# Kernel tuning notes

Measured on AMD Instinct MI355X. Metric: run time of the kernel, lower is better.

Reference implementation:

```python
import jax, jax.numpy as jnp
import numpy as np

BN_EPS = 1e-5


def setup_inputs() -> dict:
    key = jax.random.key(0)
    k1, k2, k3 = jax.random.split(key, 3)
    n, d = 4096, 128
    x = jax.random.normal(k1, (2 * n, d), dtype=jnp.float32)
    affinity_A = jax.random.normal(k2, (n, n), dtype=jnp.float32)
    # Xavier-uniform-like init for the [d, d] weight
    lim = float(np.sqrt(6.0 / (d + d)))
    weight = jax.random.uniform(k3, (d, d), dtype=jnp.float32, minval=-lim, maxval=lim)
    gamma = jnp.ones((d,), dtype=jnp.float32)
    beta = jnp.zeros((d,), dtype=jnp.float32)
    return {"x": x, "affinity_A": affinity_A, "weight": weight, "gamma": gamma, "beta": beta}


def reference(x, affinity_A, weight, gamma, beta):
    # Binarize affinity
    A = jnp.where(affinity_A > 0, 1.0, 0.0).astype(x.dtype)  # [n, n]
    n = A.shape[0]
    I = jnp.eye(n, dtype=x.dtype)
    # Block adjacency [[A, I], [I, A]] -> [2n, 2n]
    adj = jnp.block([[A, I], [I, A]])
    # Symmetric normalization D^{-1/2} A D^{-1/2}.
    # (Original code materializes D^{-1/2} as a full matrix and does two O(n^3)
    # matmuls; mathematically it is just row/column scaling, done here directly.)
    deg = adj.sum(axis=1)                 # [2n], >= 1 because of identity blocks
    dinv = deg ** -0.5
    norm_A = dinv[:, None] * adj * dinv[None, :]
    # GCN propagation: (norm_A @ x) @ W
    h = (norm_A @ x) @ weight             # [2n, d]
    # BatchNorm1d (training mode, biased variance) + ReLU
    mean = h.mean(axis=0)
    var = h.var(axis=0)
    h = (h - mean) * jax.lax.rsqrt(var + BN_EPS) * gamma + beta
    return jax.nn.relu(h)
```

## Files before the change

### kernel.cpp

```cpp
#include <hip/hip_runtime.h>
#include <stdint.h>


#define N_NODES 4096
#define D 128
#define TWO_N (2*N_NODES)

typedef unsigned short u16;
typedef __bf16 bf16;
typedef bf16 bf16x8 __attribute__((ext_vector_type(8)));
typedef float f32x4 __attribute__((ext_vector_type(4)));
typedef u16 u16x8 __attribute__((ext_vector_type(8)));

__device__ __forceinline__ float bf2f(u16 u) {
    return __builtin_bit_cast(float, ((unsigned)u) << 16);
}
__device__ __forceinline__ u16 f2bf(float f) {
    unsigned b = __builtin_bit_cast(unsigned, f);
    unsigned r = (b + 0x7FFFu + ((b >> 16) & 1u)) >> 16;
    return (u16)r;
}
__device__ __forceinline__ bool det_fp32(const u16* gamma) {
    return gamma[0] != (u16)0x3F80;
}

__global__ void k_degscale(const void* __restrict__ x, const void* __restrict__ aff,
                           const void* __restrict__ W, const u16* __restrict__ gamma,
                           float* __restrict__ dinv, u16* __restrict__ XsT,
                           u16* __restrict__ WT) {
    int t = threadIdx.x;
    bool fp32 = det_fp32(gamma);
    const u16* W16 = (const u16*)W;
    const float* W32 = (const float*)W;

    if (blockIdx.x >= 256) {
        int o = (blockIdx.x - 256) * 16 + (t >> 4);
        int cg = (t & 15) * 8;
        u16x8 wv;
        #pragma unroll
        for (int e = 0; e < 8; ++e) {
            size_t wi = (size_t)(cg + e) * D + o;
            float v = fp32 ? W32[wi] : bf2f(W16[wi]);
            wv[e] = f2bf(v);
        }
        *reinterpret_cast<u16x8*>(WT + (size_t)o * D + cg) = wv;
        return;
    }

    __shared__ int scnt[16];
    __shared__ float sdinv[16];
    int wid = t >> 6, lane = t & 63;
    int j0 = blockIdx.x * 16;

    int cnt[4] = {0, 0, 0, 0};
    if (!fp32) {
        const u16* base = (const u16*)aff + (size_t)(j0 + wid * 4) * N_NODES;
        #pragma unroll
        for (int r = 0; r < 4; ++r)
            #pragma unroll
            for (int k = 0; k < 8; ++k) {
                u16x8 v = *reinterpret_cast<const u16x8*>(base + (size_t)r * N_NODES + k * 512 + lane * 8);
                #pragma unroll
                for (int e = 0; e < 8; ++e) cnt[r] += ((short)v[e] > 0) ? 1 : 0;
            }
    } else {
        const float* base = (const float*)aff + (size_t)(j0 + wid * 4) * N_NODES;
        #pragma unroll
        for (int r = 0; r < 4; ++r)
            #pragma unroll
            for (int k = 0; k < 16; ++k) {
                f32x4 v = *reinterpret_cast<const f32x4*>(base + (size_t)r * N_NODES + k * 256 + lane * 4);
                #pragma unroll
                for (int e = 0; e < 4; ++e) cnt[r] += (v[e] > 0.f) ? 1 : 0;
            }
    }
    #pragma unroll
    for (int r = 0; r < 4; ++r) {
        int c = cnt[r];
        #pragma unroll
        for (int off = 32; off; off >>= 1) c += __shfl_down(c, off, 64);
        if (lane == 0) scnt[wid * 4 + r] = c;
    }
    __syncthreads();
    if (t < 16) {
        float d = rsqrtf((float)(scnt[t] + 1));
        sdinv[t] = d;
        dinv[j0 + t] = d;
    }
    __syncthreads();

    int cc = t & 127;
    const u16* xb16 = (const u16*)x + ((t < 128) ? (size_t)0 : (size_t)N_NODES * D);
    const float* xb32 = (const float*)x + ((t < 128) ? (size_t)0 : (size_t)N_NODES * D);
    u16x8 b0, b1;
    #pragma unroll
    for (int jl = 0; jl < 8; ++jl) {
        size_t xi = (size_t)(j0 + jl) * D + cc;
        float xv = fp32 ? xb32[xi] : bf2f(xb16[xi]);
        b0[jl] = f2bf(sdinv[jl] * xv);
    }
    #pragma unroll
    for (int jl = 0; jl < 8; ++jl) {
        size_t xi = (size_t)(j0 + 8 + jl) * D + cc;
        float xv = fp32 ? xb32[xi] : bf2f(xb16[xi]);
        b1[jl] = f2bf(sdinv[8 + jl] * xv);
    }
    *reinterpret_cast<u16x8*>(XsT + (size_t)t * N_NODES + j0) = b0;
    *reinterpret_cast<u16x8*>(XsT + (size_t)t * N_NODES + j0 + 8) = b1;
}

#define BM 32
#define BN 256
#define BK 64
#define SK 4
#define KCHUNK (N_NODES / SK)
#define LDSS 68

__launch_bounds__(256, 2)
__global__ void k_gemm(const void* __restrict__ aff, const u16* __restrict__ XsT,
                       const u16* __restrict__ gamma, u16* __restrict__ Ypart) {
    __shared__ u16 sA[BM * LDSS];
    __shared__ u16 sB[BN * LDSS];
    int tid = threadIdx.x;
    bool fp32 = det_fp32(gamma);
    int mt = blockIdx.x >> 2;
    int sk = blockIdx.x & 3;
    int rm0 = mt * BM;
    int kk0 = sk * KCHUNK;
    int lane = tid & 63, wid = tid >> 6;
    int quad = lane >> 4, l15 = lane & 15;

    f32x4 acc[2][4];
    #pragma unroll
    for (int i = 0; i < 2; ++i)
        #pragma unroll
        for (int j = 0; j < 4; ++j) acc[i][j] = (f32x4){0.f, 0.f, 0.f, 0.f};

    int arow = tid >> 3;
    int acol = (tid & 7) * 8;
    const u16* agp16 = (const u16*)aff + (size_t)(rm0 + arow) * N_NODES + kk0 + acol;
    const float* agp32 = (const float*)aff + (size_t)(rm0 + arow) * N_NODES + kk0 + acol;
    int brow0 = tid >> 3;
    int bcol = (tid & 7) * 8;
    const u16* bgp = XsT + (size_t)brow0 * N_NODES + kk0 + bcol;

    u16x8 pa16; f32x4 pa32a, pa32b;
    u16x8 pb[8];

    if (!fp32) pa16 = *reinterpret_cast<const u16x8*>(agp16);
    else { pa32a = *reinterpret_cast<const f32x4*>(agp32); pa32b = *reinterpret_cast<const f32x4*>(agp32 + 4); }
    #pragma unroll
    for (int p = 0; p < 8; ++p)
        pb[p] = *reinterpret_cast<const u16x8*>(bgp + (size_t)p * 32 * N_NODES);

    for (int kk = 0; kk < KCHUNK / BK; ++kk) {
        u16x8 ab;
        if (!fp32) {
            #pragma unroll
            for (int e = 0; e < 8; ++e) ab[e] = ((short)pa16[e] > 0) ? (u16)0x3F80 : (u16)0;
        } else {
            #pragma unroll
            for (int e = 0; e < 4; ++e) {
                ab[e]     = (pa32a[e] > 0.f) ? (u16)0x3F80 : (u16)0;
                ab[4 + e] = (pa32b[e] > 0.f) ? (u16)0x3F80 : (u16)0;
            }
        }
        __syncthreads();
        *reinterpret_cast<u16x8*>(sA + arow * LDSS + acol) = ab;
        #pragma unroll
        for (int p = 0; p < 8; ++p)
            *reinterpret_cast<u16x8*>(sB + (p * 32 + brow0) * LDSS + bcol) = pb[p];
        __syncthreads();

        if (kk < KCHUNK / BK - 1) {
            int off = (kk + 1) * BK;
            if (!fp32) pa16 = *reinterpret_cast<const u16x8*>(agp16 + off);
            else { pa32a = *reinterpret_cast<const f32x4*>(agp32 + off); pa32b = *reinterpret_cast<const f32x4*>(agp32 + off + 4); }
            #pragma unroll
            for (int p = 0; p < 8; ++p)
                pb[p] = *reinterpret_cast<const u16x8*>(bgp + (size_t)p * 32 * N_NODES + off);
        }

        #pragma unroll
        for (int ks = 0; ks < 2; ++ks) {
            bf16x8 af0 = *reinterpret_cast<const bf16x8*>(sA + l15 * LDSS + ks * 32 + quad * 8);
            bf16x8 af1 = *reinterpret_cast<const bf16x8*>(sA + (16 + l15) * LDSS + ks * 32 + quad * 8);
            #pragma unroll
            for (int j = 0; j < 4; ++j) {
                bf16x8 bfr = *reinterpret_cast<const bf16x8*>(sB + (wid * 64 + j * 16 + l15) * LDSS + ks * 32 + quad * 8);
                acc[0][j] = __builtin_amdgcn_mfma_f32_16x16x32_bf16(af0, bfr, acc[0][j], 0, 0, 0);
                acc[1][j] = __builtin_amdgcn_mfma_f32_16x16x32_bf16(af1, bfr, acc[1][j], 0, 0, 0);
            }
        }
    }

    u16* yp = Ypart + (size_t)sk * N_NODES * 256;
    #pragma unroll
    for (int i = 0; i < 2; ++i) {
        int row = rm0 + i * 16 + quad * 4;
        #pragma unroll
        for (int j = 0; j < 4; ++j) {
            int col = wid * 64 + j * 16 + l15;
            #pragma unroll
            for (int r = 0; r < 4; ++r)
                yp[(size_t)(row + r) * 256 + col] = f2bf(acc[i][j][r]);
        }
    }
}

__global__ void k_comb(const u16* __restrict__ Ypart, const void* __restrict__ x,
                       const u16* __restrict__ WT, const u16* __restrict__ gamma,
                       const float* __restrict__ dinv, u16* __restrict__ hpre,
                       float* __restrict__ pS, float* __restrict__ pQ) {
    __shared__ u16 sH[32 * 136];
    __shared__ u16 sWT[128 * 136];
    __shared__ float sOut[32 * 132];
    int t = threadIdx.x;
    bool fp32 = det_fp32(gamma);
    int r0 = blockIdx.x * 32;
    bool top = blockIdx.x < 128;
    int node0 = top ? r0 : r0 - N_NODES;
    const u16* x16 = (const u16*)x;
    const float* x32 = (const float*)x;

    #pragma unroll
    for (int p = 0; p < 2; ++p) {
        int r = (t >> 4) + p * 16;
        int c0 = (t & 15) * 8;
        int node = node0 + r;
        int ycol = (top ? 0 : 128) + c0;
        float fs[8] = {0.f, 0.f, 0.f, 0.f, 0.f, 0.f, 0.f, 0.f};
        #pragma unroll
        for (int sk = 0; sk < SK; ++sk) {
            u16x8 yv = *reinterpret_cast<const u16x8*>(Ypart + ((size_t)sk * N_NODES + node) * 256 + ycol);
            #pragma unroll
            for (int e = 0; e < 8; ++e) fs[e] += bf2f(yv[e]);
        }
        float dv = dinv[node];
        size_t xi = (top ? (size_t)(N_NODES + node) : (size_t)node) * D + c0;
        u16x8 hv;
        if (!fp32) {
            u16x8 xv = *reinterpret_cast<const u16x8*>(x16 + xi);
            #pragma unroll
            for (int e = 0; e < 8; ++e) hv[e] = f2bf(dv * fs[e] + dv * dv * bf2f(xv[e]));
        } else {
            f32x4 xa = *reinterpret_cast<const f32x4*>(x32 + xi);
            f32x4 xb = *reinterpret_cast<const f32x4*>(x32 + xi + 4);
            #pragma unroll
            for (int e = 0; e < 4; ++e) {
                hv[e]     = f2bf(dv * fs[e]     + dv * dv * xa[e]);
                hv[4 + e] = f2bf(dv * fs[4 + e] + dv * dv * xb[e]);
            }
        }
        *reinterpret_cast<u16x8*>(sH + r * 136 + c0) = hv;
    }
    #pragma unroll
    for (int p = 0; p < 8; ++p) {
        int idx = p * 256 + t;
        int o = idx >> 4;
        int cg = (idx & 15) * 8;
        u16x8 wv = *reinterpret_cast<const u16x8*>(WT + (size_t)o * D + cg);
        *reinterpret_cast<u16x8*>(sWT + o * 136 + cg) = wv;
    }
    __syncthreads();

    int lane = t & 63, wid = t >> 6;
    int wm = wid >> 1, wn = wid & 1;
    int quad = lane >> 4, l15 = lane & 15;
    f32x4 acc[4];
    #pragma unroll
    for (int j = 0; j < 4; ++j) acc[j] = (f32x4){0.f, 0.f, 0.f, 0.f};
    #pragma unroll
    for (int ks = 0; ks < 4; ++ks) {
        bf16x8 af = *reinterpret_cast<const bf16x8*>(sH + (wm * 16 + l15) * 136 + ks * 32 + quad * 8);
        #pragma unroll
        for (int j = 0; j < 4; ++j) {
            bf16x8 bfr = *reinterpret_cast<const bf16x8*>(sWT + (wn * 64 + j * 16 + l15) * 136 + ks * 32 + quad * 8);
            acc[j] = __builtin_amdgcn_mfma_f32_16x16x32_bf16(af, bfr, acc[j], 0, 0, 0);
        }
    }
    #pragma unroll
    for (int j = 0; j < 4; ++j) {
        int row = wm * 16 + quad * 4;
        int col = wn * 64 + j * 16 + l15;
        #pragma unroll
        for (int r = 0; r < 4; ++r) sOut[(row + r) * 132 + col] = acc[j][r];
    }
    __syncthreads();
    #pragma unroll
    for (int p = 0; p < 16; ++p) {
        int idx = p * 256 + t;
        int r = idx >> 7, c = idx & 127;
        hpre[(size_t)(r0 + r) * D + c] = f2bf(sOut[r * 132 + c]);
    }
    if (t < 128) {
        float s = 0.f, q = 0.f;
        #pragma unroll
        for (int r = 0; r < 32; ++r) {
            float v = sOut[r * 132 + t];
            s += v; q += v * v;
        }
        pS[blockIdx.x * 128 + t] = s;
        pQ[blockIdx.x * 128 + t] = q;
    }
}

__global__ void k_stats(const float* __restrict__ pS, const float* __restrict__ pQ,
                        const void* __restrict__ gamma, const void* __restrict__ beta,
                        const u16* __restrict__ gdet, float* __restrict__ scsh) {
    __shared__ float rs[256], rq[256];
    int t = threadIdx.x;
    int c0 = blockIdx.x * 8;
    int cl = t & 7;
    int rr = t >> 3;
    float s = 0.f, q = 0.f;
    #pragma unroll
    for (int i = 0; i < 8; ++i) {
        int row = rr + i * 32;
        s += pS[row * 128 + c0 + cl];
        q += pQ[row * 128 + c0 + cl];
    }
    rs[t] = s; rq[t] = q;
    __syncthreads();
    #pragma unroll
    for (int st = 128; st >= 8; st >>= 1) {
        if (t < st) { rs[t] += rs[t + st]; rq[t] += rq[t + st]; }
        __syncthreads();
    }
    if (t < 8) {
        bool fp32 = det_fp32(gdet);
        int c = c0 + t;
        float mean = rs[t] * (1.0f / TWO_N);
        float var = fmaxf(rq[t] * (1.0f / TWO_N) - mean * mean, 0.f);
        float inv = rsqrtf(var + 1e-5f);
        float g = fp32 ? ((const float*)gamma)[c] : bf2f(((const u16*)gamma)[c]);
        float b = fp32 ? ((const float*)beta)[c]  : bf2f(((const u16*)beta)[c]);
        scsh[c] = inv * g;
        scsh[128 + c] = b - mean * inv * g;
    }
}

__global__ void k_bn(const u16* __restrict__ hpre, const float* __restrict__ scsh,
                     const u16* __restrict__ gdet, void* __restrict__ out) {
    __shared__ float ssc[128], ssh[128];
    int t = threadIdx.x;
    bool fp32 = det_fp32(gdet);
    if (t < 128) { ssc[t] = scsh[t]; ssh[t] = scsh[128 + t]; }
    __syncthreads();
    size_t base = (size_t)blockIdx.x * 2048 + t * 8;
    int c0 = (t & 15) * 8;
    u16x8 hv = *reinterpret_cast<const u16x8*>(hpre + base);
    if (!fp32) {
        u16x8 ov;
        #pragma unroll
        for (int e = 0; e < 8; ++e) {
            float v = bf2f(hv[e]) * ssc[c0 + e] + ssh[c0 + e];
            ov[e] = f2bf(fmaxf(v, 0.f));
        }
        *reinterpret_cast<u16x8*>((u16*)out + base) = ov;
    } else {
        float* o = (float*)out + base;
        #pragma unroll
        for (int e = 0; e < 8; ++e) {
            float v = bf2f(hv[e]) * ssc[c0 + e] + ssh[c0 + e];
            o[e] = fmaxf(v, 0.f);
        }
    }
}

extern "C" void kernel_launch(void* const* d_in, const int* in_sizes, int n_in,
                              void* d_out, int out_size, void* d_ws, size_t ws_size,
                              hipStream_t stream) {
    const void* x = d_in[0];
    const void* aff = d_in[1];
    const void* W = d_in[2];
    const u16* gamma = (const u16*)d_in[3];
    const void* beta = d_in[4];

    char* ws = (char*)d_ws;
    u16* XsT = (u16*)ws;
    u16* hpre = XsT;
    u16* Ypart = (u16*)(ws + 2097152);
    float* dinv = (float*)(ws + 10485760);
    float* pS = (float*)(ws + 10502144);
    float* pQ = (float*)(ws + 10633216);
    float* scsh = (float*)(ws + 10764288);
    u16* WT = (u16*)(ws + 10765312);

    k_degscale<<<264, 256, 0, stream>>>(x, aff, W, gamma, dinv, XsT, WT);
    k_gemm<<<512, 256, 0, stream>>>(aff, XsT, gamma, Ypart);
    k_comb<<<256, 256, 0, stream>>>(Ypart, x, WT, gamma, dinv, hpre, pS, pQ);
    k_stats<<<16, 256, 0, stream>>>(pS, pQ, gamma, beta, gamma, scsh);
    k_bn<<<512, 256, 0, stream>>>(hpre, scsh, gamma, d_out);
}
```

Measured before the change: 136.3 us.

## Bit-pack binarized affinity in degree pass and feed GEMM from bitmask

The degree kernel now writes the binarized affinity as a packed bitmask and stores the scaled X in an MFMA-fragment-ready layout. The GEMM reads 1 bit per adjacency entry instead of re-reading the full fp32/bf16 matrix, expands bits to bf16 in LDS, and loads B fragments directly from global into registers. It also uses a larger 64-row tile and double-buffered LDS with register prefetch. This cuts the GEMM's global traffic on the large affinity matrix. The cost is an extra bitmask write in the first pass, fewer blocks (256) with occupancy 1, and higher register pressure.

```diff
diff --git a/kernel.cpp b/kernel.cpp
--- a/kernel.cpp
+++ b/kernel.cpp
@@ -7,6 +7,7 @@
 #define TWO_N (2*N_NODES)
 
 typedef unsigned short u16;
+typedef unsigned int u32;
 typedef __bf16 bf16;
 typedef bf16 bf16x8 __attribute__((ext_vector_type(8)));
 typedef float f32x4 __attribute__((ext_vector_type(4)));
@@ -27,7 +28,7 @@
 __global__ void k_degscale(const void* __restrict__ x, const void* __restrict__ aff,
                            const void* __restrict__ W, const u16* __restrict__ gamma,
                            float* __restrict__ dinv, u16* __restrict__ XsT,
-                           u16* __restrict__ WT) {
+                           u16* __restrict__ WT, unsigned char* __restrict__ Abits) {
     int t = threadIdx.x;
     bool fp32 = det_fp32(gamma);
     const u16* W16 = (const u16*)W;
@@ -56,23 +57,37 @@
     if (!fp32) {
         const u16* base = (const u16*)aff + (size_t)(j0 + wid * 4) * N_NODES;
         #pragma unroll
-        for (int r = 0; r < 4; ++r)
-            #pragma unroll
-            for (int k = 0; k < 8; ++k) {
-                u16x8 v = *reinterpret_cast<const u16x8*>(base + (size_t)r * N_NODES + k * 512 + lane * 8);
+        for (int r = 0; r < 4; ++r) {
+            unsigned char* ab = Abits + (size_t)(j0 + wid * 4 + r) * 512 + lane;
+            #pragma unroll
+            for (int it = 0; it < 8; ++it) {
+                u16x8 v = *reinterpret_cast<const u16x8*>(base + (size_t)r * N_NODES + it * 512 + lane * 8);
+                unsigned bb = 0;
                 #pragma unroll
-                for (int e = 0; e < 8; ++e) cnt[r] += ((short)v[e] > 0) ? 1 : 0;
+                for (int e = 0; e < 8; ++e) bb |= ((short)v[e] > 0) ? (1u << e) : 0u;
+                cnt[r] += __builtin_popcount(bb);
+                ab[it * 64] = (unsigned char)bb;
             }
+        }
     } else {
         const float* base = (const float*)aff + (size_t)(j0 + wid * 4) * N_NODES;
         #pragma unroll
-        for (int r = 0; r < 4; ++r)
-            #pragma unroll
-            for (int k = 0; k < 16; ++k) {
-                f32x4 v = *reinterpret_cast<const f32x4*>(base + (size_t)r * N_NODES + k * 256 + lane * 4);
+        for (int r = 0; r < 4; ++r) {
+            unsigned char* ab = Abits + (size_t)(j0 + wid * 4 + r) * 512 + lane;
+            #pragma unroll
+            for (int it = 0; it < 8; ++it) {
+                f32x4 va = *reinterpret_cast<const f32x4*>(base + (size_t)r * N_NODES + it * 512 + lane * 8);
+                f32x4 vb = *reinterpret_cast<const f32x4*>(base + (size_t)r * N_NODES + it * 512 + lane * 8 + 4);
+                unsigned bb = 0;
                 #pragma unroll
-                for (int e = 0; e < 4; ++e) cnt[r] += (v[e] > 0.f) ? 1 : 0;
+                for (int e = 0; e < 4; ++e) {
+                    bb |= (va[e] > 0.f) ? (1u << e) : 0u;
+                    bb |= (vb[e] > 0.f) ? (1u << (4 + e)) : 0u;
+                }
+                cnt[r] += __builtin_popcount(bb);
+                ab[it * 64] = (unsigned char)bb;
             }
+        }
     }
     #pragma unroll
     for (int r = 0; r < 4; ++r) {
@@ -105,98 +120,113 @@
         float xv = fp32 ? xb32[xi] : bf2f(xb16[xi]);
         b1[jl] = f2bf(sdinv[8 + jl] * xv);
     }
-    *reinterpret_cast<u16x8*>(XsT + (size_t)t * N_NODES + j0) = b0;
-    *reinterpret_cast<u16x8*>(XsT + (size_t)t * N_NODES + j0 + 8) = b1;
-}
-
-#define BM 32
-#define BN 256
-#define BK 64
+    int kb = j0 >> 5, qd = (j0 >> 3) & 3, cg = t >> 4, r15 = t & 15;
+    size_t idx0 = (((size_t)kb * 16 + cg) * 64 + qd * 16 + r15) * 8;
+    *reinterpret_cast<u16x8*>(XsT + idx0) = b0;
+    *reinterpret_cast<u16x8*>(XsT + idx0 + 128) = b1;
+}
+
 #define SK 4
 #define KCHUNK (N_NODES / SK)
-#define LDSS 68
-
-__launch_bounds__(256, 2)
-__global__ void k_gemm(const void* __restrict__ aff, const u16* __restrict__ XsT,
-                       const u16* __restrict__ gamma, u16* __restrict__ Ypart) {
-    __shared__ u16 sA[BM * LDSS];
-    __shared__ u16 sB[BN * LDSS];
+#define LDA 72
+
+#define PREFB(KK, PBV)                                                              \
+    {                                                                               \
+        _Pragma("unroll")                                                           \
+        for (int ks = 0; ks < 2; ++ks) {                                            \
+            _Pragma("unroll")                                                       \
+            for (int j = 0; j < 4; ++j)                                             \
+                PBV[ks * 4 + j] = *reinterpret_cast<const u16x8*>(                  \
+                    pB0 + ((KK) * 2 + ks) * 8192 + j * 512);                        \
+        }                                                                           \
+    }
+
+#define MFMA_PHASE(BUF, PBV)                                                        \
+    {                                                                               \
+        _Pragma("unroll")                                                           \
+        for (int ks = 0; ks < 2; ++ks) {                                            \
+            bf16x8 af[4];                                                           \
+            _Pragma("unroll")                                                       \
+            for (int i = 0; i < 4; ++i)                                             \
+                af[i] = *reinterpret_cast<const bf16x8*>(                           \
+                    &sA[BUF][(i * 16 + l15) * LDA + ks * 32 + quad * 8]);           \
+            _Pragma("unroll")                                                       \
+            for (int j = 0; j < 4; ++j) {                                           \
+                bf16x8 bfr = __builtin_bit_cast(bf16x8, PBV[ks * 4 + j]);           \
+                _Pragma("unroll")                                                   \
+                for (int i = 0; i < 4; ++i)                                         \
+                    acc[i][j] = __builtin_amdgcn_mfma_f32_16x16x32_bf16(            \
+                        af[i], bfr, acc[i][j], 0, 0, 0);                            \
+            }                                                                       \
+        }                                                                           \
+    }
+
+__launch_bounds__(256, 1)
+__global__ void k_gemm(const unsigned char* __restrict__ Abits, const u16* __restrict__ XsT,
+                       u16* __restrict__ Ypart) {
+    __shared__ unsigned char sBits[64 * 128];
+    __shared__ u16 sA[2][64 * LDA];
     int tid = threadIdx.x;
-    bool fp32 = det_fp32(gamma);
     int mt = blockIdx.x >> 2;
     int sk = blockIdx.x & 3;
-    int rm0 = mt * BM;
-    int kk0 = sk * KCHUNK;
+    int rm0 = mt * 64;
     int lane = tid & 63, wid = tid >> 6;
     int quad = lane >> 4, l15 = lane & 15;
 
-    f32x4 acc[2][4];
-    #pragma unroll
-    for (int i = 0; i < 2; ++i)
+    f32x4 acc[4][4];
+    #pragma unroll
+    for (int i = 0; i < 4; ++i)
         #pragma unroll
         for (int j = 0; j < 4; ++j) acc[i][j] = (f32x4){0.f, 0.f, 0.f, 0.f};
 
-    int arow = tid >> 3;
-    int acol = (tid & 7) * 8;
-    const u16* agp16 = (const u16*)aff + (size_t)(rm0 + arow) * N_NODES + kk0 + acol;
-    const float* agp32 = (const float*)aff + (size_t)(rm0 + arow) * N_NODES + kk0 + acol;
-    int brow0 = tid >> 3;
-    int bcol = (tid & 7) * 8;
-    const u16* bgp = XsT + (size_t)brow0 * N_NODES + kk0 + bcol;
-
-    u16x8 pa16; f32x4 pa32a, pa32b;
-    u16x8 pb[8];
-
-    if (!fp32) pa16 = *reinterpret_cast<const u16x8*>(agp16);
-    else { pa32a = *reinterpret_cast<const f32x4*>(agp32); pa32b = *reinterpret_cast<const f32x4*>(agp32 + 4); }
-    #pragma unroll
-    for (int p = 0; p < 8; ++p)
-        pb[p] = *reinterpret_cast<const u16x8*>(bgp + (size_t)p * 32 * N_NODES);
-
-    for (int kk = 0; kk < KCHUNK / BK; ++kk) {
-        u16x8 ab;
-        if (!fp32) {
-            #pragma unroll
-            for (int e = 0; e < 8; ++e) ab[e] = ((short)pa16[e] > 0) ? (u16)0x3F80 : (u16)0;
-        } else {
-            #pragma unroll
-            for (int e = 0; e < 4; ++e) {
-                ab[e]     = (pa32a[e] > 0.f) ? (u16)0x3F80 : (u16)0;
-                ab[4 + e] = (pa32b[e] > 0.f) ? (u16)0x3F80 : (u16)0;
-            }
-        }
+    {
+        int r = tid >> 2, seg = tid & 3;
+        const unsigned char* g = Abits + (size_t)(rm0 + r) * 512 + sk * 128 + seg * 32;
+        u16x8 lo = *reinterpret_cast<const u16x8*>(g);
+        u16x8 hi = *reinterpret_cast<const u16x8*>(g + 16);
+        int swz = (r & 7) << 4;
+        *reinterpret_cast<u16x8*>(sBits + r * 128 + ((seg * 32) ^ swz)) = lo;
+        *reinterpret_cast<u16x8*>(sBits + r * 128 + ((seg * 32 + 16) ^ swz)) = hi;
+    }
+
+    int er = tid & 63, eq = tid >> 6;
+    int eswz = (er & 7) << 4;
+    auto expand = [&](int kk, int buf) {
+        u16 w = *reinterpret_cast<const u16*>(sBits + er * 128 + (((kk << 3) + eq * 2) ^ eswz));
+        u32 out[8];
+        #pragma unroll
+        for (int m = 0; m < 8; ++m)
+            out[m] = ((w >> (2 * m)) & 1u) * 0x3F80u
+                   | (u32)((w >> (2 * m + 1)) & 1u) * 0x3F800000u;
+        *reinterpret_cast<u16x8*>(&sA[buf][er * LDA + eq * 16]) =
+            *reinterpret_cast<u16x8*>(&out[0]);
+        *reinterpret_cast<u16x8*>(&sA[buf][er * LDA + eq * 16 + 8]) =
+            *reinterpret_cast<u16x8*>(&out[4]);
+    };
+
+    const u16* pB0 = XsT + (((size_t)sk * 512 + wid * 4) * 64 + lane) * 8;
+
+    u16x8 pbA[8], pbB[8];
+    __syncthreads();
+    expand(0, 0);
+    PREFB(0, pbA);
+
+    for (int kk = 0; kk < 16; kk += 2) {
         __syncthreads();
-        *reinterpret_cast<u16x8*>(sA + arow * LDSS + acol) = ab;
-        #pragma unroll
-        for (int p = 0; p < 8; ++p)
-            *reinterpret_cast<u16x8*>(sB + (p * 32 + brow0) * LDSS + bcol) = pb[p];
+        PREFB(kk + 1, pbB);
+        expand(kk + 1, 1);
+        MFMA_PHASE(0, pbA);
         __syncthreads();
-
-        if (kk < KCHUNK / BK - 1) {
-            int off = (kk + 1) * BK;
-            if (!fp32) pa16 = *reinterpret_cast<const u16x8*>(agp16 + off);
-            else { pa32a = *reinterpret_cast<const f32x4*>(agp32 + off); pa32b = *reinterpret_cast<const f32x4*>(agp32 + off + 4); }
-            #pragma unroll
-            for (int p = 0; p < 8; ++p)
-                pb[p] = *reinterpret_cast<const u16x8*>(bgp + (size_t)p * 32 * N_NODES + off);
-        }
-
-        #pragma unroll
-        for (int ks = 0; ks < 2; ++ks) {
-            bf16x8 af0 = *reinterpret_cast<const bf16x8*>(sA + l15 * LDSS + ks * 32 + quad * 8);
-            bf16x8 af1 = *reinterpret_cast<const bf16x8*>(sA + (16 + l15) * LDSS + ks * 32 + quad * 8);
-            #pragma unroll
-            for (int j = 0; j < 4; ++j) {
-                bf16x8 bfr = *reinterpret_cast<const bf16x8*>(sB + (wid * 64 + j * 16 + l15) * LDSS + ks * 32 + quad * 8);
-                acc[0][j] = __builtin_amdgcn_mfma_f32_16x16x32_bf16(af0, bfr, acc[0][j], 0, 0, 0);
-                acc[1][j] = __builtin_amdgcn_mfma_f32_16x16x32_bf16(af1, bfr, acc[1][j], 0, 0, 0);
-            }
-        }
+        if (kk + 2 < 16) {
+            PREFB(kk + 2, pbA);
+            expand(kk + 2, 0);
+        }
+        MFMA_PHASE(1, pbB);
     }
 
     u16* yp = Ypart + (size_t)sk * N_NODES * 256;
     #pragma unroll
-    for (int i = 0; i < 2; ++i) {
+    for (int i = 0; i < 4; ++i) {
         int row = rm0 + i * 16 + quad * 4;
         #pragma unroll
         for (int j = 0; j < 4; ++j) {
@@ -386,9 +416,10 @@
     float* pQ = (float*)(ws + 10633216);
     float* scsh = (float*)(ws + 10764288);
     u16* WT = (u16*)(ws + 10765312);
-
-    k_degscale<<<264, 256, 0, stream>>>(x, aff, W, gamma, dinv, XsT, WT);
-    k_gemm<<<512, 256, 0, stream>>>(aff, XsT, gamma, Ypart);
+    unsigned char* Abits = (unsigned char*)(ws + 10798080);
+
+    k_degscale<<<264, 256, 0, stream>>>(x, aff, W, gamma, dinv, XsT, WT, Abits);
+    k_gemm<<<256, 256, 0, stream>>>(Abits, XsT, Ypart);
     k_comb<<<256, 256, 0, stream>>>(Ypart, x, WT, gamma, dinv, hpre, pS, pQ);
     k_stats<<<16, 256, 0, stream>>>(pS, pQ, gamma, beta, gamma, scsh);
     k_bn<<<512, 256, 0, stream>>>(hpre, scsh, gamma, d_out);
```

Result: faster. 133.1 us (-2.4%).
